# Kernel optimization log

Measured on AMD Instinct MI355X. Metric: run time of the kernel, lower is better.

## Reference

```python
import jax, jax.numpy as jnp
import numpy as np
from jax import lax

# RelationSimplestBlock(dim=256, heads=8): k_dim=v_dim=256, DV=32 per head, hidden=4*dim=1024.
B, N, D = 8, 1024, 256
H, DV = 8, 32
KD = D            # k_dim
HID = 4 * D       # RN hidden dim


def _ln(t, g, b, eps=1e-5):
    m = jnp.mean(t, axis=-1, keepdims=True)
    v = jnp.mean((t - m) ** 2, axis=-1, keepdims=True)  # biased var (torch LayerNorm)
    return (t - m) * lax.rsqrt(v + eps) * g + b


def setup_inputs() -> dict:
    key = jax.random.key(0)
    ks = jax.random.split(key, 6)
    std = 0.02
    return {
        'x': jax.random.normal(ks[0], (B, N, D), jnp.float32),
        'w_q': jax.random.normal(ks[1], (D, KD // H), jnp.float32) * std,   # impartial q head
        'w_kv': jax.random.normal(ks[2], (D, KD + D), jnp.float32) * std,
        'ln_out_g': jnp.ones((D,), jnp.float32),
        'ln_out_b': jnp.zeros((D,), jnp.float32),
        'ln_rel_g': jnp.ones((DV,), jnp.float32),
        'ln_rel_b': jnp.zeros((DV,), jnp.float32),
        'w_down': jax.random.normal(ks[3], (D, DV), jnp.float32) * std,
        'b_down': jnp.zeros((DV,), jnp.float32),
        'w_inner': jax.random.normal(ks[4], (2 * DV, HID), jnp.float32) * std,
        'b_inner': jnp.zeros((HID,), jnp.float32),
        'w_outer': jax.random.normal(ks[5], (HID, D), jnp.float32) * std,
        'b_outer': jnp.zeros((D,), jnp.float32),
    }


def reference(x, w_q, w_kv, ln_out_g, ln_out_b, ln_rel_g, ln_rel_b,
              w_down, b_down, w_inner, b_inner, w_outer, b_outer):
    pre = _ln(x, ln_out_g, ln_out_b)                                   # [B,N,D]
    # Relation (training branch): shared single query head (impartial_q_head)
    q = pre @ w_q                                                      # [B,N,DV]
    kv = pre @ w_kv                                                    # [B,N,KD+D]
    k = kv[..., :KD].reshape(B, N, H, DV).transpose(0, 2, 1, 3)        # [B,H,N,DV]
    v = kv[..., KD:].reshape(B, N, H, DV).transpose(0, 2, 1, 3)        # [B,H,N,DV]
    scores = jnp.einsum('bid,bhjd->bhij', q * (DV ** -0.5), k)         # [B,H,N,N]
    w = jax.nn.softmax(scores, axis=-1)
    soft = jnp.einsum('bhij,bhjd->bhid', w, v)                         # soft attention
    idx = jnp.argmax(w, axis=-1)                                       # [B,H,N] hard select
    hard = jnp.take_along_axis(v, jnp.broadcast_to(idx[..., None], (B, H, N, DV)), axis=2)
    rtn = soft - lax.stop_gradient(soft - hard)                        # straight-through
    rel = rtn.transpose(0, 2, 1, 3).reshape(B * N, H, DV)              # head-wise objects
    head_wise = _ln(rel, ln_rel_g, ln_rel_b)
    residual = (x @ w_down + b_down).reshape(B * N, 1, DV)             # downsampled context
    # RN (inner_depth=0, outer_depth=0): pair each head with the single context object
    pairs = jnp.concatenate([head_wise, jnp.broadcast_to(residual, (B * N, H, DV))], -1)
    inner = pairs @ w_inner + b_inner                                  # [BN,H,HID]
    mid = jax.nn.gelu(inner.sum(axis=1), approximate=False)            # sum over pairs
    out = mid @ w_outer + b_outer                                      # [BN,D]
    return out.reshape(B, N, D) + x
```

## Files before the change

kernel.cpp:

```cpp
#include <hip/hip_runtime.h>
#include <math.h>

#define D_    256
#define N_    1024
#define B_    8
#define H_    8
#define DV_   32
#define HID_  1024
#define ROWS_ (B_*N_)

typedef _Float16 f16;
typedef __attribute__((ext_vector_type(8))) _Float16 f16x8;
typedef __attribute__((ext_vector_type(4))) _Float16 f16x4;
typedef __attribute__((ext_vector_type(8))) short s16x8;
typedef __attribute__((ext_vector_type(4))) float f32x4;

#define LO_SCALE   2048.0f
#define INV_LO     (1.0f/2048.0f)
#define INV_LO2    (1.0f/4194304.0f)

__device__ __forceinline__ unsigned short f2bf(float f) {
    unsigned u = __float_as_uint(f);
    unsigned r = (u + 0x7fffu + ((u >> 16) & 1u)) >> 16;
    return (unsigned short)r;
}
__device__ __forceinline__ float bf2f(unsigned short u) {
    return __uint_as_float((unsigned)u << 16);
}

__device__ __forceinline__ float erf_fast(float x) {
    float ax = fabsf(x);
    float t = 1.f / (1.f + 0.3275911f * ax);
    float y = ((((1.061405429f * t - 1.453152027f) * t + 1.421413741f) * t
                - 0.284496736f) * t + 0.254829592f) * t;
    float e = __expf(-ax * ax);
    float r = 1.f - y * e;
    return x < 0.f ? -r : r;
}
__device__ __forceinline__ float gelu(float v) {
    return 0.5f * v * (1.f + erf_fast(v * 0.70710678118f));
}

__global__ __launch_bounds__(256) void k_ln(const float* __restrict__ x,
        const float* __restrict__ g, const float* __restrict__ b,
        float* __restrict__ pre, unsigned short* __restrict__ pbf) {
    int t = threadIdx.x;
    int lane = t & 63;
    int row = blockIdx.x * 4 + (t >> 6);
    const float4 v = ((const float4*)(x + row * D_))[lane];
    float s  = v.x + v.y + v.z + v.w;
    float sq = v.x*v.x + v.y*v.y + v.z*v.z + v.w*v.w;
    #pragma unroll
    for (int o = 32; o; o >>= 1) { s += __shfl_xor(s, o); sq += __shfl_xor(sq, o); }
    float m   = s * (1.0f / D_);
    float var = sq * (1.0f / D_) - m * m;
    float rs  = rsqrtf(var + 1e-5f);
    const float4 gv = ((const float4*)g)[lane];
    const float4 bv = ((const float4*)b)[lane];
    float4 o;
    o.x = (v.x - m) * rs * gv.x + bv.x;
    o.y = (v.y - m) * rs * gv.y + bv.y;
    o.z = (v.z - m) * rs * gv.z + bv.z;
    o.w = (v.w - m) * rs * gv.w + bv.w;
    ((float4*)(pre + row * D_))[lane] = o;
    ushort4 u4;
    u4.x = f2bf(o.x); u4.y = f2bf(o.y); u4.z = f2bf(o.z); u4.w = f2bf(o.w);
    *(ushort4*)(pbf + (size_t)row * D_ + lane * 4) = u4;
}

__global__ __launch_bounds__(256) void k_gemm(const float* __restrict__ A,
        const float* __restrict__ Bm, const float* __restrict__ bias,
        float* __restrict__ C, int Ncols) {
    __shared__ float As[16][64];
    __shared__ float Bs[16][64];
    int t = threadIdx.x;
    int nBase = blockIdx.x * 64, rowBase = blockIdx.y * 64;
    int tx = t & 15, ty = t >> 4;
    int arow = t >> 2, ak = (t & 3) * 4;
    int bk = t >> 4, bn = (t & 15) * 4;
    float acc[4][4] = {};
    for (int kt = 0; kt < 256; kt += 16) {
        float4 av = *(const float4*)(A + (rowBase + arow) * 256 + kt + ak);
        As[ak+0][arow] = av.x; As[ak+1][arow] = av.y;
        As[ak+2][arow] = av.z; As[ak+3][arow] = av.w;
        float4 bv = make_float4(0.f, 0.f, 0.f, 0.f);
        if (nBase + bn < Ncols)
            bv = *(const float4*)(Bm + (kt + bk) * Ncols + nBase + bn);
        *(float4*)&Bs[bk][bn] = bv;
        __syncthreads();
        #pragma unroll
        for (int kk = 0; kk < 16; ++kk) {
            float4 a4 = *(const float4*)&As[kk][ty*4];
            float4 b4 = *(const float4*)&Bs[kk][tx*4];
            acc[0][0] += a4.x*b4.x; acc[0][1] += a4.x*b4.y; acc[0][2] += a4.x*b4.z; acc[0][3] += a4.x*b4.w;
            acc[1][0] += a4.y*b4.x; acc[1][1] += a4.y*b4.y; acc[1][2] += a4.y*b4.z; acc[1][3] += a4.y*b4.w;
            acc[2][0] += a4.z*b4.x; acc[2][1] += a4.z*b4.y; acc[2][2] += a4.z*b4.z; acc[2][3] += a4.z*b4.w;
            acc[3][0] += a4.w*b4.x; acc[3][1] += a4.w*b4.y; acc[3][2] += a4.w*b4.z; acc[3][3] += a4.w*b4.w;
        }
        __syncthreads();
    }
    int col = nBase + tx * 4;
    if (col < Ncols) {
        float4 bb = make_float4(0.f,0.f,0.f,0.f);
        if (bias) bb = *(const float4*)(bias + col);
        #pragma unroll
        for (int i = 0; i < 4; ++i) {
            float4 o;
            o.x = acc[i][0] + bb.x; o.y = acc[i][1] + bb.y;
            o.z = acc[i][2] + bb.z; o.w = acc[i][3] + bb.w;
            *(float4*)(C + (rowBase + ty*4 + i) * Ncols + col) = o;
        }
    }
}

__global__ __launch_bounds__(256) void k_gemmK(const float* __restrict__ A,
        const float* __restrict__ Bm, f16* __restrict__ khi, f16* __restrict__ klo) {
    __shared__ float As[16][64];
    __shared__ float Bs[16][64];
    int t = threadIdx.x;
    int nBase = blockIdx.x * 64, rowBase = blockIdx.y * 64;
    int tx = t & 15, ty = t >> 4;
    int arow = t >> 2, ak = (t & 3) * 4;
    int bk = t >> 4, bn = (t & 15) * 4;
    float acc[4][4] = {};
    for (int kt = 0; kt < 256; kt += 16) {
        float4 av = *(const float4*)(A + (rowBase + arow) * 256 + kt + ak);
        As[ak+0][arow] = av.x; As[ak+1][arow] = av.y;
        As[ak+2][arow] = av.z; As[ak+3][arow] = av.w;
        float4 bv = *(const float4*)(Bm + (size_t)(kt + bk) * 512 + nBase + bn);
        *(float4*)&Bs[bk][bn] = bv;
        __syncthreads();
        #pragma unroll
        for (int kk = 0; kk < 16; ++kk) {
            float4 a4 = *(const float4*)&As[kk][ty*4];
            float4 b4 = *(const float4*)&Bs[kk][tx*4];
            acc[0][0] += a4.x*b4.x; acc[0][1] += a4.x*b4.y; acc[0][2] += a4.x*b4.z; acc[0][3] += a4.x*b4.w;
            acc[1][0] += a4.y*b4.x; acc[1][1] += a4.y*b4.y; acc[1][2] += a4.y*b4.z; acc[1][3] += a4.y*b4.w;
            acc[2][0] += a4.z*b4.x; acc[2][1] += a4.z*b4.y; acc[2][2] += a4.z*b4.z; acc[2][3] += a4.z*b4.w;
            acc[3][0] += a4.w*b4.x; acc[3][1] += a4.w*b4.y; acc[3][2] += a4.w*b4.z; acc[3][3] += a4.w*b4.w;
        }
        __syncthreads();
    }
    int col = nBase + tx * 4;
    #pragma unroll
    for (int i = 0; i < 4; ++i) {
        int row = rowBase + ty * 4 + i;
        f16x4 hv, lv;
        #pragma unroll
        for (int c = 0; c < 4; ++c) {
            float v = acc[i][c];
            f16 h = (f16)v;
            hv[c] = h;
            lv[c] = (f16)((v - (float)h) * LO_SCALE);
        }
        *(f16x4*)(khi + (size_t)row * 256 + col) = hv;
        *(f16x4*)(klo + (size_t)row * 256 + col) = lv;
    }
}

__global__ __launch_bounds__(256) void k_gemmV(const unsigned short* __restrict__ A,
        const unsigned short* __restrict__ Bt, unsigned short* __restrict__ V) {
    __shared__ __align__(16) unsigned short As[2][4096];
    __shared__ __align__(16) unsigned short Bs[2][4096];
    int t = threadIdx.x;
    int rowBase = blockIdx.x * 64, colBase = blockIdx.y * 64;
    int l = t & 63, w = t >> 6, wr = w >> 1, wc = w & 1;
    int r0 = t >> 3,        c0 = t & 7;
    int r1 = (t + 256) >> 3, c1 = t & 7;
    int s0 = (r0 * 8 + (c0 ^ (r0 & 7))) * 8;
    int s1 = (r1 * 8 + (c1 ^ (r1 & 7))) * 8;
    f32x4 acc00 = {0.f,0.f,0.f,0.f}, acc01 = acc00, acc10 = acc00, acc11 = acc00;
    int m = l & 15, g = l >> 4;
    int swm = m & 7;
    {
        uint4 va0 = *(const uint4*)(A  + (size_t)(rowBase + r0) * 256 + c0 * 8);
        uint4 va1 = *(const uint4*)(A  + (size_t)(rowBase + r1) * 256 + c1 * 8);
        uint4 vb0 = *(const uint4*)(Bt + (size_t)(colBase + r0) * 256 + c0 * 8);
        uint4 vb1 = *(const uint4*)(Bt + (size_t)(colBase + r1) * 256 + c1 * 8);
        *(uint4*)&As[0][s0] = va0; *(uint4*)&As[0][s1] = va1;
        *(uint4*)&Bs[0][s0] = vb0; *(uint4*)&Bs[0][s1] = vb1;
    }
    __syncthreads();
    int cur = 0;
    for (int kt = 0; kt < 4; ++kt) {
        uint4 va0, va1, vb0, vb1;
        bool pf = (kt + 1) < 4;
        if (pf) {
            int k0 = (kt + 1) * 64;
            va0 = *(const uint4*)(A  + (size_t)(rowBase + r0) * 256 + k0 + c0 * 8);
            va1 = *(const uint4*)(A  + (size_t)(rowBase + r1) * 256 + k0 + c1 * 8);
            vb0 = *(const uint4*)(Bt + (size_t)(colBase + r0) * 256 + k0 + c0 * 8);
            vb1 = *(const uint4*)(Bt + (size_t)(colBase + r1) * 256 + k0 + c1 * 8);
        }
        #pragma unroll
        for (int ks = 0; ks < 2; ++ks) {
            int kc = ks * 4 + g;
            int sc = kc ^ swm;
            s16x8 a0 = *(const s16x8*)&As[cur][((wr*32      + m) * 8 + sc) * 8];
            s16x8 a1 = *(const s16x8*)&As[cur][((wr*32 + 16 + m) * 8 + sc) * 8];
            s16x8 b0 = *(const s16x8*)&Bs[cur][((wc*32      + m) * 8 + sc) * 8];
            s16x8 b1 = *(const s16x8*)&Bs[cur][((wc*32 + 16 + m) * 8 + sc) * 8];
            acc00 = __builtin_amdgcn_mfma_f32_16x16x32_bf16(a0, b0, acc00, 0, 0, 0);
            acc01 = __builtin_amdgcn_mfma_f32_16x16x32_bf16(a0, b1, acc01, 0, 0, 0);
            acc10 = __builtin_amdgcn_mfma_f32_16x16x32_bf16(a1, b0, acc10, 0, 0, 0);
            acc11 = __builtin_amdgcn_mfma_f32_16x16x32_bf16(a1, b1, acc11, 0, 0, 0);
        }
        if (pf) {
            *(uint4*)&As[cur ^ 1][s0] = va0; *(uint4*)&As[cur ^ 1][s1] = va1;
            *(uint4*)&Bs[cur ^ 1][s0] = vb0; *(uint4*)&Bs[cur ^ 1][s1] = vb1;
        }
        __syncthreads();
        cur ^= 1;
    }
    #pragma unroll
    for (int fr = 0; fr < 2; ++fr) {
        #pragma unroll
        for (int fc = 0; fc < 2; ++fc) {
            f32x4 Acc = fr == 0 ? (fc == 0 ? acc00 : acc01)
                                : (fc == 0 ? acc10 : acc11);
            int col = colBase + wc * 32 + fc * 16 + m;
            #pragma unroll
            for (int rr = 0; rr < 4; ++rr) {
                int row = rowBase + wr * 32 + fr * 16 + g * 4 + rr;
                V[(size_t)row * 256 + col] = f2bf(Acc[rr]);
            }
        }
    }
}

__global__ __launch_bounds__(256) void k_argmax(const float* __restrict__ q,
        const f16* __restrict__ khi_g, const f16* __restrict__ klo_g,
        int* __restrict__ idx) {
    __shared__ f16x8 KH[4][128];
    __shared__ f16x8 KL[4][128];
    int t = threadIdx.x;
    int bid = blockIdx.x;
    int itile = bid >> 6, grp = bid & 63;
    int h = grp & 7, b = grp >> 3;
    int i0 = itile * 64;
    int w = t >> 6, l = t & 63, m = l & 15, g = l >> 4;
    f16x8 qh, ql;
    {
        const float* qp = q + (size_t)(b * N_ + i0 + w * 16 + m) * 32 + g * 8;
        #pragma unroll
        for (int kk = 0; kk < 8; ++kk) {
            float v = qp[kk];
            f16 hi = (f16)v;
            qh[kk] = hi;
            ql[kk] = (f16)((v - (float)hi) * LO_SCALE);
        }
    }
    int js = t >> 1, cp = t & 1;
    const uint4* gh = (const uint4*)(khi_g + (size_t)(b * N_) * 256 + h * 32);
    const uint4* gl = (const uint4*)(klo_g + (size_t)(b * N_) * 256 + h * 32);
    uint4 u0h, u1h, u0l, u1l;
    {
        int r = js * 32 + cp * 2;
        u0h = gh[r]; u1h = gh[r + 1]; u0l = gl[r]; u1l = gl[r + 1];
    }
    float best[4] = {-3e38f, -3e38f, -3e38f, -3e38f};
    int   bj[4]   = {0, 0, 0, 0};
    for (int ch = 0; ch < 8; ++ch) {
        if (ch) __syncthreads();
        *(uint4*)&KH[cp * 2    ][js] = u0h;
        *(uint4*)&KH[cp * 2 + 1][js] = u1h;
        *(uint4*)&KL[cp * 2    ][js] = u0l;
        *(uint4*)&KL[cp * 2 + 1][js] = u1l;
        __syncthreads();
        if (ch < 7) {
            int r = ((ch + 1) * 128 + js) * 32 + cp * 2;
            u0h = gh[r]; u1h = gh[r + 1]; u0l = gl[r]; u1l = gl[r + 1];
        }
        int jb = ch * 128;
        #pragma unroll
        for (int jt = 0; jt < 8; ++jt) {
            int jl = jt * 16 + m;
            f16x8 bh = KH[g][jl];
            f16x8 bl = KL[g][jl];
            f32x4 ah = {0.f, 0.f, 0.f, 0.f};
            f32x4 ax = ah, al = ah;
            ah = __builtin_amdgcn_mfma_f32_16x16x32_f16(qh, bh, ah, 0, 0, 0);
            ax = __builtin_amdgcn_mfma_f32_16x16x32_f16(qh, bl, ax, 0, 0, 0);
            ax = __builtin_amdgcn_mfma_f32_16x16x32_f16(ql, bh, ax, 0, 0, 0);
            al = __builtin_amdgcn_mfma_f32_16x16x32_f16(ql, bl, al, 0, 0, 0);
            int jg = jb + jl;
            #pragma unroll
            for (int r = 0; r < 4; ++r) {
                float s = ah[r] + ax[r] * INV_LO + al[r] * INV_LO2;
                if (s > best[r]) { best[r] = s; bj[r] = jg; }
            }
        }
    }
    #pragma unroll
    for (int off = 1; off < 16; off <<= 1) {
        #pragma unroll
        for (int r = 0; r < 4; ++r) {
            float ov = __shfl_xor(best[r], off);
            int   oj = __shfl_xor(bj[r], off);
            if (ov > best[r] || (ov == best[r] && oj < bj[r])) {
                best[r] = ov; bj[r] = oj;
            }
        }
    }
    if (m == 0) {
        #pragma unroll
        for (int r = 0; r < 4; ++r)
            idx[(b * H_ + h) * N_ + i0 + w * 16 + g * 4 + r] = bj[r];
    }
}

__global__ __launch_bounds__(256) void k_hsum(const unsigned short* __restrict__ vbf,
        const int* __restrict__ idx, const float* __restrict__ res,
        const float* __restrict__ g, const float* __restrict__ bb,
        unsigned short* __restrict__ u) {
    __shared__ float rel[32][8][33];
    int t = threadIdx.x;
    int rowBase = blockIdx.x * 32;
    int rw = t >> 3, h = t & 7;
    int bn = rowBase + rw;
    int b = bn >> 10, i = bn & 1023;
    int j = idx[(b * H_ + h) * N_ + i];
    const uint4* src = (const uint4*)(vbf + (size_t)(b * N_ + j) * 256 + h * 32);
    float v[32];
    #pragma unroll
    for (int c = 0; c < 4; ++c) {
        uint4 uu = src[c];
        v[c*8+0] = bf2f((unsigned short)(uu.x & 0xffff));
        v[c*8+1] = bf2f((unsigned short)(uu.x >> 16));
        v[c*8+2] = bf2f((unsigned short)(uu.y & 0xffff));
        v[c*8+3] = bf2f((unsigned short)(uu.y >> 16));
        v[c*8+4] = bf2f((unsigned short)(uu.z & 0xffff));
        v[c*8+5] = bf2f((unsigned short)(uu.z >> 16));
        v[c*8+6] = bf2f((unsigned short)(uu.w & 0xffff));
        v[c*8+7] = bf2f((unsigned short)(uu.w >> 16));
    }
    float s = 0.f, sq = 0.f;
    #pragma unroll
    for (int d = 0; d < 32; ++d) { s += v[d]; sq += v[d]*v[d]; }
    float m = s * (1.f/32.f), var = sq * (1.f/32.f) - m * m;
    float rs = rsqrtf(var + 1e-5f);
    #pragma unroll
    for (int d = 0; d < 32; ++d)
        rel[rw][h][d] = (v[d] - m) * rs * g[d] + bb[d];
    __syncthreads();
    #pragma unroll
    for (int e = t; e < 1024; e += 256) {
        int r = e >> 5, d = e & 31;
        float acc = 0.f;
        #pragma unroll
        for (int hh = 0; hh < 8; ++hh) acc += rel[r][hh][d];
        u[(rowBase + r) * 64 + d]      = f2bf(acc);
        u[(rowBase + r) * 64 + 32 + d] = f2bf(8.f * res[(rowBase + r) * 32 + d]);
    }
}

__global__ __launch_bounds__(256) void k_cvtT(const float* __restrict__ src,
        unsigned short* __restrict__ dst, int srcCols, int dstCols) {
    __shared__ float t64[64][65];
    int t = threadIdx.x;
    int r0 = blockIdx.x * 64, c0 = blockIdx.y * 64;
    #pragma unroll
    for (int e = t; e < 4096; e += 256) {
        int r = e >> 6, c = e & 63;
        t64[r][c] = src[(size_t)(r0 + r) * srcCols + c0 + c];
    }
    __syncthreads();
    #pragma unroll
    for (int e = t; e < 4096; e += 256) {
        int c = e >> 6, r = e & 63;
        dst[(size_t)(c0 + c) * dstCols + r0 + r] = f2bf(t64[r][c]);
    }
}

__global__ __launch_bounds__(256) void k_mid(const unsigned short* __restrict__ u,
        const unsigned short* __restrict__ wiT, const float* __restrict__ b_inner,
        unsigned short* __restrict__ mid) {
    __shared__ __align__(16) unsigned short As[4096];
    __shared__ __align__(16) unsigned short Bs[4096];
    int t = threadIdx.x;
    int rowBase = blockIdx.x * 64, colBase = blockIdx.y * 64;
    int l = t & 63, w = t >> 6, wr = w >> 1, wc = w & 1;
    int r = t >> 2, cA = (t & 3) * 2;
    {
        uint4 a0 = *(const uint4*)(u   + (size_t)(rowBase + r) * 64 + cA * 8);
        uint4 a1 = *(const uint4*)(u   + (size_t)(rowBase + r) * 64 + cA * 8 + 8);
        uint4 b0 = *(const uint4*)(wiT + (size_t)(colBase + r) * 64 + cA * 8);
        uint4 b1 = *(const uint4*)(wiT + (size_t)(colBase + r) * 64 + cA * 8 + 8);
        *(uint4*)&As[(r * 8 + ( cA      ^ (r & 7))) * 8] = a0;
        *(uint4*)&As[(r * 8 + ((cA + 1) ^ (r & 7))) * 8] = a1;
        *(uint4*)&Bs[(r * 8 + ( cA      ^ (r & 7))) * 8] = b0;
        *(uint4*)&Bs[(r * 8 + ((cA + 1) ^ (r & 7))) * 8] = b1;
    }
    __syncthreads();
    f32x4 acc00 = {0.f,0.f,0.f,0.f}, acc01 = acc00, acc10 = acc00, acc11 = acc00;
    int m = l & 15, g = l >> 4;
    int swm = m & 7;
    #pragma unroll
    for (int ks = 0; ks < 2; ++ks) {
        int kc = ks * 4 + g;
        int sc = kc ^ swm;
        s16x8 a0 = *(const s16x8*)&As[((wr*32      + m) * 8 + sc) * 8];
        s16x8 a1 = *(const s16x8*)&As[((wr*32 + 16 + m) * 8 + sc) * 8];
        s16x8 b0 = *(const s16x8*)&Bs[((wc*32      + m) * 8 + sc) * 8];
        s16x8 b1 = *(const s16x8*)&Bs[((wc*32 + 16 + m) * 8 + sc) * 8];
        acc00 = __builtin_amdgcn_mfma_f32_16x16x32_bf16(a0, b0, acc00, 0, 0, 0);
        acc01 = __builtin_amdgcn_mfma_f32_16x16x32_bf16(a0, b1, acc01, 0, 0, 0);
        acc10 = __builtin_amdgcn_mfma_f32_16x16x32_bf16(a1, b0, acc10, 0, 0, 0);
        acc11 = __builtin_amdgcn_mfma_f32_16x16x32_bf16(a1, b1, acc11, 0, 0, 0);
    }
    #pragma unroll
    for (int fr = 0; fr < 2; ++fr) {
        #pragma unroll
        for (int fc = 0; fc < 2; ++fc) {
            f32x4 A = fr == 0 ? (fc == 0 ? acc00 : acc01)
                              : (fc == 0 ? acc10 : acc11);
            int col = colBase + wc * 32 + fc * 16 + m;
            float bi = 8.f * b_inner[col];
            #pragma unroll
            for (int rr = 0; rr < 4; ++rr) {
                int row = rowBase + wr * 32 + fr * 16 + g * 4 + rr;
                mid[(size_t)row * HID_ + col] = f2bf(gelu(A[rr] + bi));
            }
        }
    }
}

__global__ __launch_bounds__(256) void k_out(const unsigned short* __restrict__ mid,
        const unsigned short* __restrict__ woT, const float* __restrict__ b_outer,
        const float* __restrict__ x, float* __restrict__ out) {
    __shared__ __align__(16) unsigned short As[2][4096];
    __shared__ __align__(16) unsigned short Bs[2][4096];
    int t = threadIdx.x;
    int rowBase = blockIdx.x * 64, colBase = blockIdx.y * 64;
    int l = t & 63, w = t >> 6, wr = w >> 1, wc = w & 1;
    int r0 = t >> 3,        c0 = t & 7;
    int r1 = (t + 256) >> 3, c1 = t & 7;
    int s0 = (r0 * 8 + (c0 ^ (r0 & 7))) * 8;
    int s1 = (r1 * 8 + (c1 ^ (r1 & 7))) * 8;
    f32x4 acc00 = {0.f,0.f,0.f,0.f}, acc01 = acc00, acc10 = acc00, acc11 = acc00;
    int m = l & 15, g = l >> 4;
    int swm = m & 7;
    {
        uint4 va0 = *(const uint4*)(mid + (size_t)(rowBase + r0) * 1024 + c0 * 8);
        uint4 va1 = *(const uint4*)(mid + (size_t)(rowBase + r1) * 1024 + c1 * 8);
        uint4 vb0 = *(const uint4*)(woT + (size_t)(colBase + r0) * 1024 + c0 * 8);
        uint4 vb1 = *(const uint4*)(woT + (size_t)(colBase + r1) * 1024 + c1 * 8);
        *(uint4*)&As[0][s0] = va0; *(uint4*)&As[0][s1] = va1;
        *(uint4*)&Bs[0][s0] = vb0; *(uint4*)&Bs[0][s1] = vb1;
    }
    __syncthreads();
    int cur = 0;
    for (int kt = 0; kt < 16; ++kt) {
        uint4 va0, va1, vb0, vb1;
        bool pf = (kt + 1) < 16;
        if (pf) {
            int k0 = (kt + 1) * 64;
            va0 = *(const uint4*)(mid + (size_t)(rowBase + r0) * 1024 + k0 + c0 * 8);
            va1 = *(const uint4*)(mid + (size_t)(rowBase + r1) * 1024 + k0 + c1 * 8);
            vb0 = *(const uint4*)(woT + (size_t)(colBase + r0) * 1024 + k0 + c0 * 8);
            vb1 = *(const uint4*)(woT + (size_t)(colBase + r1) * 1024 + k0 + c1 * 8);
        }
        #pragma unroll
        for (int ks = 0; ks < 2; ++ks) {
            int kc = ks * 4 + g;
            int sc = kc ^ swm;
            s16x8 a0 = *(const s16x8*)&As[cur][((wr*32      + m) * 8 + sc) * 8];
            s16x8 a1 = *(const s16x8*)&As[cur][((wr*32 + 16 + m) * 8 + sc) * 8];
            s16x8 b0 = *(const s16x8*)&Bs[cur][((wc*32      + m) * 8 + sc) * 8];
            s16x8 b1 = *(const s16x8*)&Bs[cur][((wc*32 + 16 + m) * 8 + sc) * 8];
            acc00 = __builtin_amdgcn_mfma_f32_16x16x32_bf16(a0, b0, acc00, 0, 0, 0);
            acc01 = __builtin_amdgcn_mfma_f32_16x16x32_bf16(a0, b1, acc01, 0, 0, 0);
            acc10 = __builtin_amdgcn_mfma_f32_16x16x32_bf16(a1, b0, acc10, 0, 0, 0);
            acc11 = __builtin_amdgcn_mfma_f32_16x16x32_bf16(a1, b1, acc11, 0, 0, 0);
        }
        if (pf) {
            *(uint4*)&As[cur ^ 1][s0] = va0; *(uint4*)&As[cur ^ 1][s1] = va1;
            *(uint4*)&Bs[cur ^ 1][s0] = vb0; *(uint4*)&Bs[cur ^ 1][s1] = vb1;
        }
        __syncthreads();
        cur ^= 1;
    }
    #pragma unroll
    for (int fr = 0; fr < 2; ++fr) {
        #pragma unroll
        for (int fc = 0; fc < 2; ++fc) {
            f32x4 A = fr == 0 ? (fc == 0 ? acc00 : acc01)
                              : (fc == 0 ? acc10 : acc11);
            int col = colBase + wc * 32 + fc * 16 + m;
            float bo = b_outer[col];
            #pragma unroll
            for (int rr = 0; rr < 4; ++rr) {
                int row = rowBase + wr * 32 + fr * 16 + g * 4 + rr;
                out[(size_t)row * 256 + col] = A[rr] + bo + x[(size_t)row * 256 + col];
            }
        }
    }
}

extern "C" void kernel_launch(void* const* d_in, const int* in_sizes, int n_in,
                              void* d_out, int out_size, void* d_ws, size_t ws_size,
                              hipStream_t stream) {
    const float* x        = (const float*)d_in[0];
    const float* w_q      = (const float*)d_in[1];
    const float* w_kv     = (const float*)d_in[2];
    const float* ln_out_g = (const float*)d_in[3];
    const float* ln_out_b = (const float*)d_in[4];
    const float* ln_rel_g = (const float*)d_in[5];
    const float* ln_rel_b = (const float*)d_in[6];
    const float* w_down   = (const float*)d_in[7];
    const float* b_down   = (const float*)d_in[8];
    const float* w_inner  = (const float*)d_in[9];
    const float* b_inner  = (const float*)d_in[10];
    const float* w_outer  = (const float*)d_in[11];
    const float* b_outer  = (const float*)d_in[12];
    float* out = (float*)d_out;

    float* ws = (float*)d_ws;
    float* pre = ws;
    unsigned short* pbf = (unsigned short*)(ws + 2097152);
    f16* khi = (f16*)(ws + 3145728);
    f16* klo = (f16*)(ws + 4194304);
    unsigned short* vbf = (unsigned short*)(ws + 5242880);
    float* qbuf   = ws + 6291456;
    float* resbuf = ws + 6553600;
    unsigned short* ubuf = (unsigned short*)(ws + 6815744);
    int* idxbuf = (int*)(ws + 7077888);
    unsigned short* woT = (unsigned short*)(ws + 7143424);
    unsigned short* wiT = (unsigned short*)(ws + 7274496);
    unsigned short* wvT = ubuf;
    unsigned short* mid = (unsigned short*)ws;

    k_ln<<<2048, 256, 0, stream>>>(x, ln_out_g, ln_out_b, pre, pbf);
    k_gemmK<<<dim3(4, 128), 256, 0, stream>>>(pre, w_kv, khi, klo);
    k_gemm<<<dim3(1, 128), 256, 0, stream>>>(pre, w_q, nullptr, qbuf, 32);
    k_gemm<<<dim3(1, 128), 256, 0, stream>>>(x, w_down, b_down, resbuf, 32);
    k_cvtT<<<dim3(4, 4), 256, 0, stream>>>(w_kv + 256, wvT, 512, 256);
    k_gemmV<<<dim3(128, 4), 256, 0, stream>>>(pbf, wvT, vbf);
    k_argmax<<<1024, 256, 0, stream>>>(qbuf, khi, klo, idxbuf);
    k_cvtT<<<dim3(16, 4), 256, 0, stream>>>(w_outer, woT, 256, 1024);
    k_cvtT<<<dim3(1, 16), 256, 0, stream>>>(w_inner, wiT, 1024, 64);
    k_hsum<<<256, 256, 0, stream>>>(vbf, idxbuf, resbuf, ln_rel_g, ln_rel_b, ubuf);
    k_mid<<<dim3(128, 16), 256, 0, stream>>>(ubuf, wiT, b_inner, mid);
    k_out<<<dim3(128, 4), 256, 0, stream>>>(mid, woT, b_outer, x, out);
}
```

Measured before the change: 149.9 us.

## Restructure argmax kernel: direct global K fragment loads, split j range across waves

The argmax kernel no longer stages K hi/lo tiles through shared memory with per-chunk barriers. Each wave now handles 32 query rows (two 16-row fragments sharing each loaded K fragment) over half of the key range. It reads K fragments straight from global memory with a one-step register prefetch, and merges the two halves through a small shared-memory reduction. This removes LDS traffic and the eight block-wide syncs and doubles B-operand reuse per load, at the cost of uncoalesced-ish global loads and more live registers. Ties between halves resolve to the lower index as before.

```diff
diff --git a/kernel.cpp b/kernel.cpp
--- a/kernel.cpp
+++ b/kernel.cpp
@@ -231,81 +231,91 @@
 __global__ __launch_bounds__(256) void k_argmax(const float* __restrict__ q,
         const f16* __restrict__ khi_g, const f16* __restrict__ klo_g,
         int* __restrict__ idx) {
-    __shared__ f16x8 KH[4][128];
-    __shared__ f16x8 KL[4][128];
+    __shared__ float mval[2][64];
+    __shared__ int   midx[2][64];
     int t = threadIdx.x;
     int bid = blockIdx.x;
     int itile = bid >> 6, grp = bid & 63;
     int h = grp & 7, b = grp >> 3;
     int i0 = itile * 64;
     int w = t >> 6, l = t & 63, m = l & 15, g = l >> 4;
-    f16x8 qh, ql;
+    int iw = w & 1, jh = w >> 1;
+    int ibase = i0 + iw * 32;
+    f16x8 qh0, ql0, qh1, ql1;
     {
-        const float* qp = q + (size_t)(b * N_ + i0 + w * 16 + m) * 32 + g * 8;
+        const float* qp0 = q + (size_t)(b * N_ + ibase + m) * 32 + g * 8;
+        const float* qp1 = qp0 + 16 * 32;
         #pragma unroll
         for (int kk = 0; kk < 8; ++kk) {
-            float v = qp[kk];
-            f16 hi = (f16)v;
-            qh[kk] = hi;
-            ql[kk] = (f16)((v - (float)hi) * LO_SCALE);
-        }
-    }
-    int js = t >> 1, cp = t & 1;
-    const uint4* gh = (const uint4*)(khi_g + (size_t)(b * N_) * 256 + h * 32);
-    const uint4* gl = (const uint4*)(klo_g + (size_t)(b * N_) * 256 + h * 32);
-    uint4 u0h, u1h, u0l, u1l;
-    {
-        int r = js * 32 + cp * 2;
-        u0h = gh[r]; u1h = gh[r + 1]; u0l = gl[r]; u1l = gl[r + 1];
-    }
-    float best[4] = {-3e38f, -3e38f, -3e38f, -3e38f};
-    int   bj[4]   = {0, 0, 0, 0};
-    for (int ch = 0; ch < 8; ++ch) {
-        if (ch) __syncthreads();
-        *(uint4*)&KH[cp * 2    ][js] = u0h;
-        *(uint4*)&KH[cp * 2 + 1][js] = u1h;
-        *(uint4*)&KL[cp * 2    ][js] = u0l;
-        *(uint4*)&KL[cp * 2 + 1][js] = u1l;
-        __syncthreads();
-        if (ch < 7) {
-            int r = ((ch + 1) * 128 + js) * 32 + cp * 2;
-            u0h = gh[r]; u1h = gh[r + 1]; u0l = gl[r]; u1l = gl[r + 1];
-        }
-        int jb = ch * 128;
-        #pragma unroll
-        for (int jt = 0; jt < 8; ++jt) {
-            int jl = jt * 16 + m;
-            f16x8 bh = KH[g][jl];
-            f16x8 bl = KL[g][jl];
-            f32x4 ah = {0.f, 0.f, 0.f, 0.f};
-            f32x4 ax = ah, al = ah;
-            ah = __builtin_amdgcn_mfma_f32_16x16x32_f16(qh, bh, ah, 0, 0, 0);
-            ax = __builtin_amdgcn_mfma_f32_16x16x32_f16(qh, bl, ax, 0, 0, 0);
-            ax = __builtin_amdgcn_mfma_f32_16x16x32_f16(ql, bh, ax, 0, 0, 0);
-            al = __builtin_amdgcn_mfma_f32_16x16x32_f16(ql, bl, al, 0, 0, 0);
-            int jg = jb + jl;
-            #pragma unroll
-            for (int r = 0; r < 4; ++r) {
-                float s = ah[r] + ax[r] * INV_LO + al[r] * INV_LO2;
-                if (s > best[r]) { best[r] = s; bj[r] = jg; }
+            float v0 = qp0[kk]; f16 h0 = (f16)v0;
+            qh0[kk] = h0; ql0[kk] = (f16)((v0 - (float)h0) * LO_SCALE);
+            float v1 = qp1[kk]; f16 h1 = (f16)v1;
+            qh1[kk] = h1; ql1[kk] = (f16)((v1 - (float)h1) * LO_SCALE);
+        }
+    }
+    const f16* ph = khi_g + (size_t)(b * N_ + jh * 512 + m) * 256 + h * 32 + g * 8;
+    const f16* pl = klo_g + (size_t)(b * N_ + jh * 512 + m) * 256 + h * 32 + g * 8;
+    float best0[4] = {-3e38f, -3e38f, -3e38f, -3e38f};
+    float best1[4] = {-3e38f, -3e38f, -3e38f, -3e38f};
+    int   bj0[4] = {0,0,0,0}, bj1[4] = {0,0,0,0};
+    f16x8 bh = *(const f16x8*)ph;
+    f16x8 bl = *(const f16x8*)pl;
+    #pragma unroll 2
+    for (int jt = 0; jt < 32; ++jt) {
+        f16x8 nh, nl;
+        if (jt < 31) {
+            nh = *(const f16x8*)(ph + (size_t)(jt + 1) * 4096);
+            nl = *(const f16x8*)(pl + (size_t)(jt + 1) * 4096);
+        }
+        f32x4 z = {0.f, 0.f, 0.f, 0.f};
+        f32x4 ah0 = __builtin_amdgcn_mfma_f32_16x16x32_f16(qh0, bh, z, 0, 0, 0);
+        f32x4 ax0 = __builtin_amdgcn_mfma_f32_16x16x32_f16(qh0, bl, z, 0, 0, 0);
+        ax0 = __builtin_amdgcn_mfma_f32_16x16x32_f16(ql0, bh, ax0, 0, 0, 0);
+        f32x4 al0 = __builtin_amdgcn_mfma_f32_16x16x32_f16(ql0, bl, z, 0, 0, 0);
+        f32x4 ah1 = __builtin_amdgcn_mfma_f32_16x16x32_f16(qh1, bh, z, 0, 0, 0);
+        f32x4 ax1 = __builtin_amdgcn_mfma_f32_16x16x32_f16(qh1, bl, z, 0, 0, 0);
+        ax1 = __builtin_amdgcn_mfma_f32_16x16x32_f16(ql1, bh, ax1, 0, 0, 0);
+        f32x4 al1 = __builtin_amdgcn_mfma_f32_16x16x32_f16(ql1, bl, z, 0, 0, 0);
+        int jg = jh * 512 + jt * 16 + m;
+        #pragma unroll
+        for (int r = 0; r < 4; ++r) {
+            float s0 = ah0[r] + ax0[r] * INV_LO + al0[r] * INV_LO2;
+            if (s0 > best0[r]) { best0[r] = s0; bj0[r] = jg; }
+            float s1 = ah1[r] + ax1[r] * INV_LO + al1[r] * INV_LO2;
+            if (s1 > best1[r]) { best1[r] = s1; bj1[r] = jg; }
+        }
+        bh = nh; bl = nl;
+    }
+    #pragma unroll
+    for (int off = 1; off < 16; off <<= 1) {
+        #pragma unroll
+        for (int r = 0; r < 4; ++r) {
+            float ov = __shfl_xor(best0[r], off);
+            int   oj = __shfl_xor(bj0[r], off);
+            if (ov > best0[r] || (ov == best0[r] && oj < bj0[r])) {
+                best0[r] = ov; bj0[r] = oj;
             }
-        }
-    }
-    #pragma unroll
-    for (int off = 1; off < 16; off <<= 1) {
+            float ov1 = __shfl_xor(best1[r], off);
+            int   oj1 = __shfl_xor(bj1[r], off);
+            if (ov1 > best1[r] || (ov1 == best1[r] && oj1 < bj1[r])) {
+                best1[r] = ov1; bj1[r] = oj1;
+            }
+        }
+    }
+    if (m == 0) {
         #pragma unroll
         for (int r = 0; r < 4; ++r) {
-            float ov = __shfl_xor(best[r], off);
-            int   oj = __shfl_xor(bj[r], off);
-            if (ov > best[r] || (ov == best[r] && oj < bj[r])) {
-                best[r] = ov; bj[r] = oj;
-            }
-        }
-    }
-    if (m == 0) {
-        #pragma unroll
-        for (int r = 0; r < 4; ++r)
-            idx[(b * H_ + h) * N_ + i0 + w * 16 + g * 4 + r] = bj[r];
+            mval[jh][iw * 32 + g * 4 + r]      = best0[r];
+            midx[jh][iw * 32 + g * 4 + r]      = bj0[r];
+            mval[jh][iw * 32 + 16 + g * 4 + r] = best1[r];
+            midx[jh][iw * 32 + 16 + g * 4 + r] = bj1[r];
+        }
+    }
+    __syncthreads();
+    if (t < 64) {
+        float v0 = mval[0][t]; int j0 = midx[0][t];
+        float v1 = mval[1][t]; int j1 = midx[1][t];
+        idx[(b * H_ + h) * N_ + i0 + t] = (v1 > v0) ? j1 : j0;
     }
 }
 
```

After: 151.5 us. No clear change (+1.1%).
